# Kernel tuning notes

Hardware: AMD Instinct MI355X
Metric: run time of the kernel (lower is better)

## Reference

```python
import jax, jax.numpy as jnp
import numpy as np

T, B = 256, 64
X_DIM, H_DIM, Z_DIM = 128, 1024, 128


def _lin(k, out_d, in_d):
    return jax.random.normal(k, (out_d, in_d), jnp.float32) * 0.05


def setup_inputs() -> dict:
    key = jax.random.key(0)
    ks = jax.random.split(key, 18)
    return {
        "x": jax.random.normal(ks[0], (T, B, X_DIM), jnp.float32),
        "y": jax.random.uniform(ks[1], (T, B, X_DIM), jnp.float32),
        "eps": jax.random.normal(ks[2], (T, B, Z_DIM), jnp.float32),
        # hidden_state_rnn: GRU(x_dim -> h_dim), bias=False
        "h_Wih": _lin(ks[3], 3 * H_DIM, X_DIM),
        "h_Whh": _lin(ks[4], 3 * H_DIM, H_DIM),
        # rnn: GRU(h_dim + x_dim -> h_dim), bias=False (input is [y_t, h_t])
        "a_Wih": _lin(ks[5], 3 * H_DIM, X_DIM + H_DIM),
        "a_Whh": _lin(ks[6], 3 * H_DIM, H_DIM),
        "enc_W1": _lin(ks[7], H_DIM, H_DIM), "enc_b1": jnp.zeros(H_DIM, jnp.float32),
        "enc_W2": _lin(ks[8], H_DIM, H_DIM), "enc_b2": jnp.zeros(H_DIM, jnp.float32),
        "encm_W": _lin(ks[9], Z_DIM, H_DIM), "encm_b": jnp.zeros(Z_DIM, jnp.float32),
        "encs_W": _lin(ks[10], Z_DIM, H_DIM), "encs_b": jnp.zeros(Z_DIM, jnp.float32),
        "pr_W": _lin(ks[11], H_DIM, H_DIM), "pr_b": jnp.zeros(H_DIM, jnp.float32),
        "prm_W": _lin(ks[12], Z_DIM, H_DIM), "prm_b": jnp.zeros(Z_DIM, jnp.float32),
        "prs_W": _lin(ks[13], Z_DIM, H_DIM), "prs_b": jnp.zeros(Z_DIM, jnp.float32),
        "dec_W1": _lin(ks[14], H_DIM, H_DIM + Z_DIM), "dec_b1": jnp.zeros(H_DIM, jnp.float32),
        "dec_W2": _lin(ks[15], H_DIM, H_DIM), "dec_b2": jnp.zeros(H_DIM, jnp.float32),
        "decm_W": _lin(ks[16], X_DIM, H_DIM), "decm_b": jnp.zeros(X_DIM, jnp.float32),
        "decs_W": _lin(ks[17], X_DIM, H_DIM), "decs_b": jnp.zeros(X_DIM, jnp.float32),
    }


def _gru(xs, Wih, Whh):
    """Single-layer PyTorch-style GRU without biases. xs: [T,B,in]. Returns [T,B,H]."""
    h0 = jnp.zeros((xs.shape[1], Whh.shape[1]), xs.dtype)
    def step(h, xt):
        gi = xt @ Wih.T                      # [B, 3H]
        gh = h @ Whh.T                       # [B, 3H]
        ir, iz, inn = jnp.split(gi, 3, axis=-1)
        hr, hz, hn = jnp.split(gh, 3, axis=-1)
        r = jax.nn.sigmoid(ir + hr)
        zg = jax.nn.sigmoid(iz + hz)
        n = jnp.tanh(inn + r * hn)
        h_new = (1.0 - zg) * n + zg * h
        return h_new, h_new
    return jax.lax.scan(step, h0, xs)[1]


def srnn_forward(x, y, eps, h_Wih, h_Whh, a_Wih, a_Whh,
                 enc_W1, enc_b1, enc_W2, enc_b2, encm_W, encm_b, encs_W, encs_b,
                 pr_W, pr_b, prm_W, prm_b, prs_W, prs_b,
                 dec_W1, dec_b1, dec_W2, dec_b2, decm_W, decm_b, decs_W, decs_b):
    h_seq = _gru(x, h_Wih, h_Whh)            # [T,B,H] forward-time states
    # NOTE: original code aliases h_list and reverses it in place, so all later
    # uses of h_list[t] actually see the time-reversed sequence. Reproduce that.
    h_rev = h_seq[::-1]
    y_rev = y[::-1]
    a_rev = _gru(jnp.concatenate([y_rev, h_rev], axis=-1), a_Wih, a_Whh)  # backward GRU
    a_fwd = a_rev[::-1]                      # a at forward time t saw steps t..T-1

    enc = jax.nn.relu(jax.nn.relu(a_fwd @ enc_W1.T + enc_b1) @ enc_W2.T + enc_b2)
    enc_mean = enc @ encm_W.T + encm_b       # [T,B,Z]
    enc_std = jax.nn.softplus(enc @ encs_W.T + encs_b)
    z = eps * enc_std + enc_mean             # reparameterized sample

    pri = jax.nn.relu(h_rev @ pr_W.T + pr_b)  # bug-faithful: reversed h
    prior_mean = pri @ prm_W.T + prm_b
    prior_std = jax.nn.softplus(pri @ prs_W.T + prs_b)

    dec = jax.nn.relu(
        jax.nn.relu(jnp.concatenate([z, h_rev], axis=-1) @ dec_W1.T + dec_b1)
        @ dec_W2.T + dec_b2)
    dec_mean = jax.nn.sigmoid(dec @ decm_W.T + decm_b)  # [T,B,X]
    dec_std = jax.nn.softplus(dec @ decs_W.T + decs_b)

    kld = 0.5 * jnp.sum(
        2.0 * jnp.log(prior_std) - 2.0 * jnp.log(enc_std)
        + (enc_std ** 2 + (enc_mean - prior_mean) ** 2) / prior_std ** 2 - 1.0)
    nll = -jnp.sum(y * jnp.log(dec_mean) + (1.0 - y) * jnp.log(1.0 - dec_mean))
    return kld, nll, enc_mean, enc_std, dec_mean, dec_std


def reference(x, y, eps, h_Wih, h_Whh, a_Wih, a_Whh,
              enc_W1, enc_b1, enc_W2, enc_b2, encm_W, encm_b, encs_W, encs_b,
              pr_W, pr_b, prm_W, prm_b, prs_W, prs_b,
              dec_W1, dec_b1, dec_W2, dec_b2, decm_W, decm_b, decs_W, decs_b):
    return srnn_forward(x, y, eps, h_Wih, h_Whh, a_Wih, a_Whh,
                        enc_W1, enc_b1, enc_W2, enc_b2, encm_W, encm_b, encs_W, encs_b,
                        pr_W, pr_b, prm_W, prm_b, prs_W, prs_b,
                        dec_W1, dec_b1, dec_W2, dec_b2, decm_W, decm_b, decs_W, decs_b)
```

## Files before the change

### kernel.cpp

```cpp
#include <hip/hip_runtime.h>
#include <cstdint>
#include <cstddef>

#define NT   256
#define NB   64
#define XD   128
#define HD   1024
#define ZD   128
#define H3   3072
#define TBM  16384

typedef __attribute__((ext_vector_type(8))) short bf16x8;
typedef __attribute__((ext_vector_type(4))) float f32x4;
typedef __attribute__((ext_vector_type(4))) unsigned int u32x4;

__device__ __forceinline__ unsigned short f2bf(float f){
  unsigned int u = __float_as_uint(f);
  u += 0x7fffu + ((u >> 16) & 1u);
  return (unsigned short)(u >> 16);
}
__device__ __forceinline__ float bf2f(unsigned short h){
  return __uint_as_float(((unsigned int)h) << 16);
}

template<int N>
__device__ __forceinline__ void vwait(){
  asm volatile("s_waitcnt vmcnt(%0)" :: "i"(N) : "memory");
  __builtin_amdgcn_sched_barrier(0);
}

__device__ __forceinline__ float fsigmoid(float x){
  return 1.f / (1.f + __expf(-x));
}
__device__ __forceinline__ float ftanh(float x){
  float xc = fminf(fmaxf(x, -15.f), 15.f);
  float e = __expf(2.f * xc);
  return (e - 1.f) / (e + 1.f);
}

__device__ __forceinline__ void wait_tags(const unsigned int* tags, unsigned int target){
  if (threadIdx.x < 64){
    const unsigned int* p = tags + threadIdx.x * 32;
    for (;;){
      unsigned int v;
      asm volatile("global_load_dword %0, %1, off sc0 sc1\n\ts_waitcnt vmcnt(0)"
                   : "=v"(v) : "v"(p) : "memory");
      if (__all((int)(v >= target))) break;
    }
  }
  __syncthreads();
}

struct CvtArgs { const float* src[17]; };

__global__ void cvt_all(CvtArgs a, unsigned short* wdst, unsigned short* xdst, unsigned short* ydst){
  const long NG = 2572288;
  for (long g = blockIdx.x*blockDim.x + threadIdx.x; g < NG; g += (long)gridDim.x*blockDim.x){
    long i = g * 8;
    const float* s; unsigned short* d;
    if      (i < 393216)  { s=a.src[0]+i;             d=wdst+i; }
    else if (i < 3538944) { s=a.src[1]+(i-393216);    d=wdst+i; }
    else if (i < 7077888) { s=a.src[2]+(i-3538944);   d=wdst+i; }
    else if (i < 10223616){ s=a.src[3]+(i-7077888);   d=wdst+i; }
    else if (i < 11272192){ s=a.src[4]+(i-10223616);  d=wdst+i; }
    else if (i < 12320768){ s=a.src[5]+(i-11272192);  d=wdst+i; }
    else if (i < 12451840){ s=a.src[6]+(i-12320768);  d=wdst+i; }
    else if (i < 12582912){ s=a.src[7]+(i-12451840);  d=wdst+i; }
    else if (i < 13631488){ s=a.src[8]+(i-12582912);  d=wdst+i; }
    else if (i < 13762560){ s=a.src[9]+(i-13631488);  d=wdst+i; }
    else if (i < 13893632){ s=a.src[10]+(i-13762560); d=wdst+i; }
    else if (i < 15073280){ s=a.src[11]+(i-13893632); d=wdst+i; }
    else if (i < 16121856){ s=a.src[12]+(i-15073280); d=wdst+i; }
    else if (i < 16252928){ s=a.src[13]+(i-16121856); d=wdst+i; }
    else if (i < 16384000){ s=a.src[14]+(i-16252928); d=wdst+i; }
    else if (i < 18481152){ s=a.src[15]+(i-16384000); d=xdst+(i-16384000); }
    else                  { s=a.src[16]+(i-18481152); d=ydst+(i-18481152); }
    float4 v0 = *(const float4*)s;
    float4 v1 = *(const float4*)(s + 4);
    u32x4 o;
    o.x = (unsigned int)f2bf(v0.x) | ((unsigned int)f2bf(v0.y) << 16);
    o.y = (unsigned int)f2bf(v0.z) | ((unsigned int)f2bf(v0.w) << 16);
    o.z = (unsigned int)f2bf(v1.x) | ((unsigned int)f2bf(v1.y) << 16);
    o.w = (unsigned int)f2bf(v1.z) | ((unsigned int)f2bf(v1.w) << 16);
    *(u32x4*)d = o;
  }
}

template<int ACT, int OUT_BF, int BIAS>
__launch_bounds__(256)
__global__ void gemm_bf16(const unsigned short* __restrict__ A1, int rev1, int K1,
                          const unsigned short* __restrict__ A2, int rev2, int K,
                          const unsigned short* __restrict__ W,
                          const float* __restrict__ bias,
                          void* __restrict__ Cv, int N, int m0)
{
  __shared__ __align__(16) unsigned short As[128][40];
  __shared__ __align__(16) unsigned short Ws[128][40];
  const int tid   = threadIdx.x;
  const int mbase = blockIdx.y * 128;
  const int nbase = blockIdx.x * 128;
  const int wid = tid >> 6, lane = tid & 63;
  const int wr = wid >> 1, wc = wid & 1;
  const int fr = lane & 15;
  const int kc = (lane >> 4) * 8;
  const int K2 = K - K1;
  const int nk = K >> 5;

  f32x4 acc[4][4];
  #pragma unroll
  for (int i = 0; i < 4; ++i)
    #pragma unroll
    for (int j = 0; j < 4; ++j)
      acc[i][j] = (f32x4){0.f, 0.f, 0.f, 0.f};

  for (int ks = 0; ks < nk; ++ks){
    const int k0 = ks << 5;
    __syncthreads();
    for (int l = tid; l < 512; l += 256){
      int row = l >> 2, c = l & 3;
      int kk = k0 + c*8;
      int m = m0 + mbase + row;
      uint4 v;
      if (kk < K1){
        int mm = rev1 ? (((255 - (m >> 6)) << 6) | (m & 63)) : m;
        v = *(const uint4*)(A1 + (size_t)mm * K1 + kk);
      } else {
        int mm = rev2 ? (((255 - (m >> 6)) << 6) | (m & 63)) : m;
        v = *(const uint4*)(A2 + (size_t)mm * K2 + (kk - K1));
      }
      *(uint4*)&As[row][c*8] = v;
    }
    for (int l = tid; l < 512; l += 256){
      int row = l >> 2, c = l & 3;
      uint4 v = *(const uint4*)(W + (size_t)(nbase + row) * K + k0 + c*8);
      *(uint4*)&Ws[row][c*8] = v;
    }
    __syncthreads();
    bf16x8 af[4], bfm[4];
    #pragma unroll
    for (int f = 0; f < 4; ++f) af[f]  = *(const bf16x8*)&As[wr*64 + f*16 + fr][kc];
    #pragma unroll
    for (int f = 0; f < 4; ++f) bfm[f] = *(const bf16x8*)&Ws[wc*64 + f*16 + fr][kc];
    #pragma unroll
    for (int i = 0; i < 4; ++i)
      #pragma unroll
      for (int j = 0; j < 4; ++j)
        acc[i][j] = __builtin_amdgcn_mfma_f32_16x16x32_bf16(af[i], bfm[j], acc[i][j], 0, 0, 0);
  }

  #pragma unroll
  for (int i = 0; i < 4; ++i){
    #pragma unroll
    for (int j = 0; j < 4; ++j){
      #pragma unroll
      for (int r = 0; r < 4; ++r){
        int row = mbase + wr*64 + i*16 + (lane >> 4)*4 + r;
        int col = nbase + wc*64 + j*16 + fr;
        float v = acc[i][j][r];
        if (BIAS) v += bias[col];
        if (ACT == 1) v = fmaxf(v, 0.f);
        else if (ACT == 2) v = 1.f / (1.f + expf(-v));
        else if (ACT == 3) v = (v > 20.f) ? v : log1pf(expf(v));
        if (OUT_BF) ((unsigned short*)Cv)[(size_t)row * N + col] = f2bf(v);
        else        ((float*)Cv)[(size_t)row * N + col] = v;
      }
    }
  }
}

__device__ void gemm_gi_tile(char* smem,
                             const unsigned short* __restrict__ A1, int rev1, int K1,
                             const unsigned short* __restrict__ A2, int rev2, int K,
                             const unsigned short* __restrict__ W,
                             unsigned short* __restrict__ C, int m0, int bx, int by)
{
  unsigned short (*As)[40] = (unsigned short(*)[40])smem;
  unsigned short (*Ws)[40] = (unsigned short(*)[40])(smem + 10240);
  const int tid   = threadIdx.x;
  const int mbase = by * 128;
  const int nbase = bx * 128;
  const int wid = tid >> 6, lane = tid & 63;
  const int wr = wid >> 1, wc = wid & 1;
  const int fr = lane & 15;
  const int kc = (lane >> 4) * 8;
  const int K2 = K - K1;
  const int nk = K >> 5;

  f32x4 acc[4][4];
  #pragma unroll
  for (int i = 0; i < 4; ++i)
    #pragma unroll
    for (int j = 0; j < 4; ++j)
      acc[i][j] = (f32x4){0.f, 0.f, 0.f, 0.f};

  for (int ks = 0; ks < nk; ++ks){
    const int k0 = ks << 5;
    __syncthreads();
    for (int l = tid; l < 512; l += 256){
      int row = l >> 2, c = l & 3;
      int kk = k0 + c*8;
      int m = m0 + mbase + row;
      uint4 v;
      if (kk < K1){
        int mm = rev1 ? (((255 - (m >> 6)) << 6) | (m & 63)) : m;
        v = *(const uint4*)(A1 + (size_t)mm * K1 + kk);
      } else {
        int mm = rev2 ? (((255 - (m >> 6)) << 6) | (m & 63)) : m;
        v = *(const uint4*)(A2 + (size_t)mm * K2 + (kk - K1));
      }
      *(uint4*)&As[row][c*8] = v;
    }
    for (int l = tid; l < 512; l += 256){
      int row = l >> 2, c = l & 3;
      uint4 v = *(const uint4*)(W + (size_t)(nbase + row) * K + k0 + c*8);
      *(uint4*)&Ws[row][c*8] = v;
    }
    __syncthreads();
    bf16x8 af[4], bfm[4];
    #pragma unroll
    for (int f = 0; f < 4; ++f) af[f]  = *(const bf16x8*)&As[wr*64 + f*16 + fr][kc];
    #pragma unroll
    for (int f = 0; f < 4; ++f) bfm[f] = *(const bf16x8*)&Ws[wc*64 + f*16 + fr][kc];
    #pragma unroll
    for (int i = 0; i < 4; ++i)
      #pragma unroll
      for (int j = 0; j < 4; ++j)
        acc[i][j] = __builtin_amdgcn_mfma_f32_16x16x32_bf16(af[i], bfm[j], acc[i][j], 0, 0, 0);
  }

  #pragma unroll
  for (int i = 0; i < 4; ++i){
    #pragma unroll
    for (int j = 0; j < 4; ++j){
      #pragma unroll
      for (int r = 0; r < 4; ++r){
        int row = mbase + wr*64 + i*16 + (lane >> 4)*4 + r;
        int col = nbase + wc*64 + j*16 + fr;
        C[(size_t)row * H3 + col] = f2bf(acc[i][j][r]);
      }
    }
  }
  __syncthreads();
}

__device__ void gru_body(char* smem,
                         const unsigned short* __restrict__ W3,
                         const unsigned short* __restrict__ gi,
                         unsigned short* __restrict__ seq,
                         float* __restrict__ hstate,
                         unsigned int* __restrict__ tags,
                         int t0, int dir, int out_off, int nsteps)
{
  uint4 (*Wf)[3][64] = (uint4(*)[3][64])smem;
  unsigned short (*hb2)[16] = (unsigned short(*)[16])(smem + 98304);
  unsigned int* scnt = (unsigned int*)(smem + 100352);
  const int tid  = threadIdx.x;
  const int bid  = blockIdx.x;
  const int c0   = bid * 16;
  const int wid  = tid >> 6, lane = tid & 63;
  const int fr   = lane & 15, q = lane >> 4;
  const int rowb = wid*16 + q*4;
  const int arow = wid*16 + fr;

  for (int ks = wid*8; ks < wid*8 + 8; ++ks)
    #pragma unroll
    for (int g = 0; g < 3; ++g)
      Wf[ks][g][lane] = *(const uint4*)(W3 + (size_t)(g*HD + c0 + fr)*HD + ks*32 + q*8);
  if (tid == 0) *scnt = 0u;

  float hc[4];
  if (t0 == 0){
    hc[0] = hc[1] = hc[2] = hc[3] = 0.f;
  } else {
    #pragma unroll
    for (int r = 0; r < 4; ++r)
      hc[r] = hstate[(size_t)(rowb + r)*HD + c0 + fr];
  }
  __syncthreads();

  for (int tt = 0; tt < nsteps; ++tt){
    const int t = t0 + tt;

    unsigned short g_ir[4], g_iz[4], g_in[4];
    {
      const unsigned short* gb = gi + (size_t)tt*NB*H3;
      #pragma unroll
      for (int r = 0; r < 4; ++r){
        const unsigned short* p = gb + (size_t)(rowb + r)*H3 + c0 + fr;
        g_ir[r] = p[0];
        g_iz[r] = p[HD];
        g_in[r] = p[2*HD];
      }
    }

    f32x4 aR = (f32x4){0.f,0.f,0.f,0.f};
    f32x4 aZ = (f32x4){0.f,0.f,0.f,0.f};
    f32x4 aN = (f32x4){0.f,0.f,0.f,0.f};

    if (t > 0){
      if (tt >= 1) wait_tags(tags, (unsigned int)tt);
      const unsigned short* hp = seq + (size_t)(out_off + dir*(t-1))*NB*HD
                                     + (size_t)arow*HD + q*8;
      u32x4 A[32];
      #pragma unroll
      for (int ks = 0; ks < 32; ++ks)
        asm volatile("global_load_dwordx4 %0, %1, off offset:%2"
                     : "=v"(A[ks]) : "v"(hp), "i"(ks*64));
      #pragma unroll
      for (int b4 = 0; b4 < 4; ++b4){
        if (b4 == 0) vwait<24>();
        else if (b4 == 1) vwait<16>();
        else if (b4 == 2) vwait<8>();
        else vwait<0>();
        #pragma unroll
        for (int k8 = 0; k8 < 8; ++k8){
          const int ks = b4*8 + k8;
          bf16x8 a = *(const bf16x8*)&A[ks];
          aR = __builtin_amdgcn_mfma_f32_16x16x32_bf16(a, *(const bf16x8*)&Wf[ks][0][lane], aR, 0, 0, 0);
          aZ = __builtin_amdgcn_mfma_f32_16x16x32_bf16(a, *(const bf16x8*)&Wf[ks][1][lane], aZ, 0, 0, 0);
          aN = __builtin_amdgcn_mfma_f32_16x16x32_bf16(a, *(const bf16x8*)&Wf[ks][2][lane], aN, 0, 0, 0);
        }
      }
    }

    #pragma unroll
    for (int r = 0; r < 4; ++r){
      float rr = fsigmoid(bf2f(g_ir[r]) + aR[r]);
      float zz = fsigmoid(bf2f(g_iz[r]) + aZ[r]);
      float nn = ftanh(bf2f(g_in[r]) + rr * aN[r]);
      hc[r] = (1.f - zz) * nn + zz * hc[r];
      hb2[rowb + r][fr] = f2bf(hc[r]);
    }
    __syncthreads();
    {
      int row = tid >> 2, c4 = (tid & 3) * 4;
      unsigned long long v = *(const unsigned long long*)&hb2[row][c4];
      unsigned long long* dst = (unsigned long long*)(seq + (size_t)(out_off + dir*t)*NB*HD
                                                          + (size_t)row*HD + c0 + c4);
      (void)__hip_atomic_exchange(dst, v, __ATOMIC_RELAXED, __HIP_MEMORY_SCOPE_AGENT);
    }
    if (tt < nsteps - 1){
      vwait<0>();
      if (lane == 0){
        unsigned int old = atomicAdd(scnt, 1u);
        if (old == (unsigned int)(4*tt + 3))
          (void)__hip_atomic_exchange(tags + bid*32, (unsigned int)(tt + 1),
                                      __ATOMIC_RELAXED, __HIP_MEMORY_SCOPE_AGENT);
      }
    }
  }

  #pragma unroll
  for (int r = 0; r < 4; ++r)
    hstate[(size_t)(rowb + r)*HD + c0 + fr] = hc[r];
}

__global__ __launch_bounds__(256, 1)
void gru_seq(const unsigned short* __restrict__ W3, const unsigned short* __restrict__ gi,
             unsigned short* __restrict__ seq, float* __restrict__ hstate,
             unsigned int* __restrict__ tags, int t0, int dir, int out_off, int nsteps)
{
  __shared__ __align__(16) char smem[100608];
  gru_body(smem, W3, gi, seq, hstate, tags, t0, dir, out_off, nsteps);
}

__global__ __launch_bounds__(256, 1)
void gru_fat(const unsigned short* __restrict__ W3, const unsigned short* __restrict__ gi,
             unsigned short* __restrict__ seq, float* __restrict__ hstate,
             unsigned int* __restrict__ tags, int t0, int dir, int out_off, int nsteps,
             const unsigned short* __restrict__ gA1, int grev1, int gK1,
             const unsigned short* __restrict__ gA2, int grev2, int gK,
             const unsigned short* __restrict__ gW, unsigned short* __restrict__ gC, int gm0)
{
  __shared__ __align__(16) char smem[100608];
  if (blockIdx.x < 64){
    gru_body(smem, W3, gi, seq, hstate, tags, t0, dir, out_off, nsteps);
  } else {
    for (int tl = blockIdx.x - 64; tl < 768; tl += 192)
      gemm_gi_tile(smem, gA1, grev1, gK1, gA2, grev2, gK, gW, gC, gm0, tl % 24, tl / 24);
  }
}

__global__ void z_make(const float* __restrict__ eps, const float* __restrict__ em,
                       const float* __restrict__ es, unsigned short* __restrict__ zb, int n){
  for (int i = blockIdx.x*blockDim.x + threadIdx.x; i < n; i += gridDim.x*blockDim.x)
    zb[i] = f2bf(eps[i] * es[i] + em[i]);
}

__global__ void kld_partial(const float* __restrict__ em, const float* __restrict__ es,
                            const float* __restrict__ pm, const float* __restrict__ ps,
                            float* __restrict__ part, int n){
  float s = 0.f;
  for (int i = blockIdx.x*blockDim.x + threadIdx.x; i < n; i += gridDim.x*blockDim.x){
    float e = es[i], p = ps[i], d = em[i] - pm[i];
    s += 2.f*(logf(p) - logf(e)) + (e*e + d*d)/(p*p) - 1.f;
  }
  __shared__ float red[256];
  red[threadIdx.x] = s; __syncthreads();
  for (int off = 128; off; off >>= 1){
    if (threadIdx.x < off) red[threadIdx.x] += red[threadIdx.x + off];
    __syncthreads();
  }
  if (threadIdx.x == 0) part[blockIdx.x] = red[0];
}

__global__ void nll_partial(const float* __restrict__ y, const float* __restrict__ dm,
                            float* __restrict__ part, int n){
  float s = 0.f;
  for (int i = blockIdx.x*blockDim.x + threadIdx.x; i < n; i += gridDim.x*blockDim.x){
    float yy = y[i], d = dm[i];
    s += yy * logf(d) + (1.f - yy) * logf(1.f - d);
  }
  __shared__ float red[256];
  red[threadIdx.x] = s; __syncthreads();
  for (int off = 128; off; off >>= 1){
    if (threadIdx.x < off) red[threadIdx.x] += red[threadIdx.x + off];
    __syncthreads();
  }
  if (threadIdx.x == 0) part[blockIdx.x] = red[0];
}

__global__ void final_sum(const float* __restrict__ part, int n, float scale, float* __restrict__ out){
  float s = 0.f;
  for (int i = threadIdx.x; i < n; i += 256) s += part[i];
  __shared__ float red[256];
  red[threadIdx.x] = s; __syncthreads();
  for (int off = 128; off; off >>= 1){
    if (threadIdx.x < off) red[threadIdx.x] += red[threadIdx.x + off];
    __syncthreads();
  }
  if (threadIdx.x == 0) out[0] = scale * red[0];
}

extern "C" void kernel_launch(void* const* d_in, const int* in_sizes, int n_in,
                              void* d_out, int out_size, void* d_ws, size_t ws_size,
                              hipStream_t stream)
{
  const float* y   = (const float*)d_in[1];
  const float* eps = (const float*)d_in[2];
  const float* enc_b1 = (const float*)d_in[8];
  const float* enc_b2 = (const float*)d_in[10];
  const float* encm_b = (const float*)d_in[12];
  const float* encs_b = (const float*)d_in[14];
  const float* pr_b   = (const float*)d_in[16];
  const float* prm_b  = (const float*)d_in[18];
  const float* prs_b  = (const float*)d_in[20];
  const float* dec_b1 = (const float*)d_in[22];
  const float* dec_b2 = (const float*)d_in[24];
  const float* decm_b = (const float*)d_in[26];
  const float* decs_b = (const float*)d_in[28];

  char* ws = (char*)d_ws;
  size_t off = 0;
  auto alloc = [&](size_t bytes){ size_t o = off; off += (bytes + 255) & ~(size_t)255; return o; };
  const size_t o_big   = alloc((size_t)71303168);
  const size_t o_hseq  = alloc((size_t)TBM * HD * 2);
  const size_t o_aseq  = alloc((size_t)TBM * HD * 2);
  const size_t o_wbf   = alloc((size_t)16384000 * 2);
  const size_t o_hst   = alloc((size_t)NB * HD * 4);
  const size_t o_bar   = alloc((size_t)65536);
  const size_t o_pkld  = alloc((size_t)1024 * 4);
  const size_t o_pnll  = alloc((size_t)1024 * 4);
  (void)off; (void)ws_size;

  char* big = ws + o_big;
  unsigned short* gihA = (unsigned short*)(big);
  unsigned short* gihB = (unsigned short*)(big + 25165824);
  unsigned short* xbf  = (unsigned short*)(big + 50331648);
  unsigned short* ybf  = (unsigned short*)(big + 54525952);
  unsigned short* tA  = (unsigned short*)(big);
  unsigned short* tB  = (unsigned short*)(big + 33554432);
  unsigned short* zbf = (unsigned short*)(big + 67108864);

  unsigned short* hseq = (unsigned short*)(ws + o_hseq);
  unsigned short* aseq = (unsigned short*)(ws + o_aseq);
  unsigned short* wbf  = (unsigned short*)(ws + o_wbf);
  float* hstate = (float*)(ws + o_hst);
  unsigned int* bar = (unsigned int*)(ws + o_bar);
  float* pkld = (float*)(ws + o_pkld);
  float* pnll = (float*)(ws + o_pnll);

  const int widx[15] = {3,4,5,6,7,9,11,13,15,17,19,21,23,25,27};
  const size_t wsz[15] = {393216,3145728,3538944,3145728,1048576,1048576,131072,131072,
                          1048576,131072,131072,1179648,1048576,131072,131072};
  size_t woff[15]; { size_t a = 0; for (int i = 0; i < 15; ++i){ woff[i] = a; a += wsz[i]; } }
  unsigned short* w_hWih = wbf + woff[0];
  unsigned short* w_hWhh = wbf + woff[1];
  unsigned short* w_aWih = wbf + woff[2];
  unsigned short* w_aWhh = wbf + woff[3];
  unsigned short* w_enc1 = wbf + woff[4];
  unsigned short* w_enc2 = wbf + woff[5];
  unsigned short* w_encm = wbf + woff[6];
  unsigned short* w_encs = wbf + woff[7];
  unsigned short* w_pr   = wbf + woff[8];
  unsigned short* w_prm  = wbf + woff[9];
  unsigned short* w_prs  = wbf + woff[10];
  unsigned short* w_dec1 = wbf + woff[11];
  unsigned short* w_dec2 = wbf + woff[12];
  unsigned short* w_decm = wbf + woff[13];
  unsigned short* w_decs = wbf + woff[14];

  float* out = (float*)d_out;
  float* em_out = out + 2;
  float* es_out = out + 2 + 2097152;
  float* dm_out = out + 2 + 2*2097152;
  float* ds_out = out + 2 + 3*2097152;
  float* pm = dm_out;
  float* ps = ds_out;

  CvtArgs ca;
  for (int i = 0; i < 15; ++i) ca.src[i] = (const float*)d_in[widx[i]];
  ca.src[15] = (const float*)d_in[0];
  ca.src[16] = (const float*)d_in[1];
  cvt_all<<<2048, 256, 0, stream>>>(ca, wbf, xbf, ybf);
  (void)hipMemsetAsync(bar, 0, 65536, stream);

  const dim3 blk(256);
  const dim3 gQ3072(24, 32);
  const dim3 g1024(HD/128, TBM/128);
  const dim3 g128(1, TBM/128);
  const unsigned short* nul = (const unsigned short*)nullptr;

  gemm_bf16<0,1,0><<<gQ3072, blk, 0, stream>>>(xbf, 0, XD, nul, 0, XD, w_hWih, nullptr, gihA, H3, 0);
  gru_fat<<<256, blk, 0, stream>>>(w_hWhh, gihA, hseq, hstate, bar + 0*2048, 0,   +1, 0, 64,
                                   xbf, 0, XD, nul, 0, XD, w_hWih, gihB, 4096);
  gru_fat<<<256, blk, 0, stream>>>(w_hWhh, gihB, hseq, hstate, bar + 1*2048, 64,  +1, 0, 64,
                                   xbf, 0, XD, nul, 0, XD, w_hWih, gihA, 8192);
  gru_fat<<<256, blk, 0, stream>>>(w_hWhh, gihA, hseq, hstate, bar + 2*2048, 128, +1, 0, 64,
                                   xbf, 0, XD, nul, 0, XD, w_hWih, gihB, 12288);
  gru_seq<<<64, blk, 0, stream>>>(w_hWhh, gihB, hseq, hstate, bar + 3*2048, 192, +1, 0, 64);

  gemm_bf16<0,1,0><<<gQ3072, blk, 0, stream>>>(ybf, 1, XD, hseq, 1, XD + HD, w_aWih, nullptr, gihA, H3, 0);
  gru_fat<<<256, blk, 0, stream>>>(w_aWhh, gihA, aseq, hstate, bar + 4*2048, 0,   -1, 255, 64,
                                   ybf, 1, XD, hseq, 1, XD + HD, w_aWih, gihB, 4096);
  gru_fat<<<256, blk, 0, stream>>>(w_aWhh, gihB, aseq, hstate, bar + 5*2048, 64,  -1, 255, 64,
                                   ybf, 1, XD, hseq, 1, XD + HD, w_aWih, gihA, 8192);
  gru_fat<<<256, blk, 0, stream>>>(w_aWhh, gihA, aseq, hstate, bar + 6*2048, 128, -1, 255, 64,
                                   ybf, 1, XD, hseq, 1, XD + HD, w_aWih, gihB, 12288);
  gru_seq<<<64, blk, 0, stream>>>(w_aWhh, gihB, aseq, hstate, bar + 7*2048, 192, -1, 255, 64);

  gemm_bf16<1,1,1><<<g1024, blk, 0, stream>>>(aseq, 0, HD, nul, 0, HD, w_enc1, enc_b1, tA, HD, 0);
  gemm_bf16<1,1,1><<<g1024, blk, 0, stream>>>(tA, 0, HD, nul, 0, HD, w_enc2, enc_b2, tB, HD, 0);
  gemm_bf16<0,0,1><<<g128, blk, 0, stream>>>(tB, 0, HD, nul, 0, HD, w_encm, encm_b, em_out, ZD, 0);
  gemm_bf16<3,0,1><<<g128, blk, 0, stream>>>(tB, 0, HD, nul, 0, HD, w_encs, encs_b, es_out, ZD, 0);
  z_make<<<2048, 256, 0, stream>>>(eps, em_out, es_out, zbf, TBM*ZD);

  gemm_bf16<1,1,1><<<g1024, blk, 0, stream>>>(hseq, 1, HD, nul, 1, HD, w_pr, pr_b, tA, HD, 0);
  gemm_bf16<0,0,1><<<g128, blk, 0, stream>>>(tA, 0, HD, nul, 0, HD, w_prm, prm_b, pm, ZD, 0);
  gemm_bf16<3,0,1><<<g128, blk, 0, stream>>>(tA, 0, HD, nul, 0, HD, w_prs, prs_b, ps, ZD, 0);
  kld_partial<<<1024, 256, 0, stream>>>(em_out, es_out, pm, ps, pkld, TBM*ZD);
  final_sum<<<1, 256, 0, stream>>>(pkld, 1024, 0.5f, out + 0);

  gemm_bf16<1,1,1><<<g1024, blk, 0, stream>>>(zbf, 0, ZD, hseq, 1, ZD + HD, w_dec1, dec_b1, tA, HD, 0);
  gemm_bf16<1,1,1><<<g1024, blk, 0, stream>>>(tA, 0, HD, nul, 0, HD, w_dec2, dec_b2, tB, HD, 0);
  gemm_bf16<2,0,1><<<g128, blk, 0, stream>>>(tB, 0, HD, nul, 0, HD, w_decm, decm_b, dm_out, ZD, 0);
  gemm_bf16<3,0,1><<<g128, blk, 0, stream>>>(tB, 0, HD, nul, 0, HD, w_decs, decs_b, ds_out, ZD, 0);

  nll_partial<<<1024, 256, 0, stream>>>(y, dm_out, pnll, TBM*XD);
  final_sum<<<1, 256, 0, stream>>>(pnll, 1024, -1.0f, out + 1);
}
```

Baseline: 4.839 ms.

## Replace tag-based GRU step barrier with sentinel-value polling on hidden state

Removes the per-block tag counters and the tag-polling barrier between GRU timesteps. Instead, the hidden sequence buffers are pre-filled with 0xFF, and each block repeatedly loads the previous step's hidden row with cache-bypassing loads until no 0xFFFF sentinel halves remain. The goal is to cut the extra round trip for tag publish and poll, and to let data arrival itself act as the signal. In exchange, it adds two large memsets, reloads the full A tile on every retry, and relies on real bf16 values never equalling the 0xFFFF pattern (a NaN encoding). It also only checks two of the eight halves per load.

New measurement: 6.321 ms. 30.6% more time.

```diff
diff --git a/kernel.cpp b/kernel.cpp
--- a/kernel.cpp
+++ b/kernel.cpp
@@ -36,19 +36,6 @@
   float xc = fminf(fmaxf(x, -15.f), 15.f);
   float e = __expf(2.f * xc);
   return (e - 1.f) / (e + 1.f);
-}
-
-__device__ __forceinline__ void wait_tags(const unsigned int* tags, unsigned int target){
-  if (threadIdx.x < 64){
-    const unsigned int* p = tags + threadIdx.x * 32;
-    for (;;){
-      unsigned int v;
-      asm volatile("global_load_dword %0, %1, off sc0 sc1\n\ts_waitcnt vmcnt(0)"
-                   : "=v"(v) : "v"(p) : "memory");
-      if (__all((int)(v >= target))) break;
-    }
-  }
-  __syncthreads();
 }
 
 struct CvtArgs { const float* src[17]; };
@@ -248,12 +235,10 @@
                          const unsigned short* __restrict__ gi,
                          unsigned short* __restrict__ seq,
                          float* __restrict__ hstate,
-                         unsigned int* __restrict__ tags,
                          int t0, int dir, int out_off, int nsteps)
 {
   uint4 (*Wf)[3][64] = (uint4(*)[3][64])smem;
   unsigned short (*hb2)[16] = (unsigned short(*)[16])(smem + 98304);
-  unsigned int* scnt = (unsigned int*)(smem + 100352);
   const int tid  = threadIdx.x;
   const int bid  = blockIdx.x;
   const int c0   = bid * 16;
@@ -266,7 +251,6 @@
     #pragma unroll
     for (int g = 0; g < 3; ++g)
       Wf[ks][g][lane] = *(const uint4*)(W3 + (size_t)(g*HD + c0 + fr)*HD + ks*32 + q*8);
-  if (tid == 0) *scnt = 0u;
 
   float hc[4];
   if (t0 == 0){
@@ -298,28 +282,29 @@
     f32x4 aN = (f32x4){0.f,0.f,0.f,0.f};
 
     if (t > 0){
-      if (tt >= 1) wait_tags(tags, (unsigned int)tt);
       const unsigned short* hp = seq + (size_t)(out_off + dir*(t-1))*NB*HD
                                      + (size_t)arow*HD + q*8;
       u32x4 A[32];
+      for (;;){
+        #pragma unroll
+        for (int ks = 0; ks < 32; ++ks)
+          asm volatile("global_load_dwordx4 %0, %1, off offset:%2 sc0 sc1"
+                       : "=v"(A[ks]) : "v"(hp), "i"(ks*64));
+        vwait<0>();
+        unsigned int bad = 0u;
+        #pragma unroll
+        for (int ks = 0; ks < 32; ++ks){
+          bad |= ((A[ks].x & 0xFFFFu) == 0xFFFFu) ? 1u : 0u;
+          bad |= ((A[ks].z & 0xFFFFu) == 0xFFFFu) ? 1u : 0u;
+        }
+        if (__all(bad == 0u)) break;
+      }
       #pragma unroll
-      for (int ks = 0; ks < 32; ++ks)
-        asm volatile("global_load_dwordx4 %0, %1, off offset:%2"
-                     : "=v"(A[ks]) : "v"(hp), "i"(ks*64));
-      #pragma unroll
-      for (int b4 = 0; b4 < 4; ++b4){
-        if (b4 == 0) vwait<24>();
-        else if (b4 == 1) vwait<16>();
-        else if (b4 == 2) vwait<8>();
-        else vwait<0>();
-        #pragma unroll
-        for (int k8 = 0; k8 < 8; ++k8){
-          const int ks = b4*8 + k8;
-          bf16x8 a = *(const bf16x8*)&A[ks];
-          aR = __builtin_amdgcn_mfma_f32_16x16x32_bf16(a, *(const bf16x8*)&Wf[ks][0][lane], aR, 0, 0, 0);
-          aZ = __builtin_amdgcn_mfma_f32_16x16x32_bf16(a, *(const bf16x8*)&Wf[ks][1][lane], aZ, 0, 0, 0);
-          aN = __builtin_amdgcn_mfma_f32_16x16x32_bf16(a, *(const bf16x8*)&Wf[ks][2][lane], aN, 0, 0, 0);
-        }
+      for (int ks = 0; ks < 32; ++ks){
+        bf16x8 a = *(const bf16x8*)&A[ks];
+        aR = __builtin_amdgcn_mfma_f32_16x16x32_bf16(a, *(const bf16x8*)&Wf[ks][0][lane], aR, 0, 0, 0);
+        aZ = __builtin_amdgcn_mfma_f32_16x16x32_bf16(a, *(const bf16x8*)&Wf[ks][1][lane], aZ, 0, 0, 0);
+        aN = __builtin_amdgcn_mfma_f32_16x16x32_bf16(a, *(const bf16x8*)&Wf[ks][2][lane], aN, 0, 0, 0);
       }
     }
 
@@ -339,15 +324,7 @@
                                                           + (size_t)row*HD + c0 + c4);
       (void)__hip_atomic_exchange(dst, v, __ATOMIC_RELAXED, __HIP_MEMORY_SCOPE_AGENT);
     }
-    if (tt < nsteps - 1){
-      vwait<0>();
-      if (lane == 0){
-        unsigned int old = atomicAdd(scnt, 1u);
-        if (old == (unsigned int)(4*tt + 3))
-          (void)__hip_atomic_exchange(tags + bid*32, (unsigned int)(tt + 1),
-                                      __ATOMIC_RELAXED, __HIP_MEMORY_SCOPE_AGENT);
-      }
-    }
+    __syncthreads();
   }
 
   #pragma unroll
@@ -358,23 +335,23 @@
 __global__ __launch_bounds__(256, 1)
 void gru_seq(const unsigned short* __restrict__ W3, const unsigned short* __restrict__ gi,
              unsigned short* __restrict__ seq, float* __restrict__ hstate,
-             unsigned int* __restrict__ tags, int t0, int dir, int out_off, int nsteps)
+             int t0, int dir, int out_off, int nsteps)
 {
   __shared__ __align__(16) char smem[100608];
-  gru_body(smem, W3, gi, seq, hstate, tags, t0, dir, out_off, nsteps);
+  gru_body(smem, W3, gi, seq, hstate, t0, dir, out_off, nsteps);
 }
 
 __global__ __launch_bounds__(256, 1)
 void gru_fat(const unsigned short* __restrict__ W3, const unsigned short* __restrict__ gi,
              unsigned short* __restrict__ seq, float* __restrict__ hstate,
-             unsigned int* __restrict__ tags, int t0, int dir, int out_off, int nsteps,
+             int t0, int dir, int out_off, int nsteps,
              const unsigned short* __restrict__ gA1, int grev1, int gK1,
              const unsigned short* __restrict__ gA2, int grev2, int gK,
              const unsigned short* __restrict__ gW, unsigned short* __restrict__ gC, int gm0)
 {
   __shared__ __align__(16) char smem[100608];
   if (blockIdx.x < 64){
-    gru_body(smem, W3, gi, seq, hstate, tags, t0, dir, out_off, nsteps);
+    gru_body(smem, W3, gi, seq, hstate, t0, dir, out_off, nsteps);
   } else {
     for (int tl = blockIdx.x - 64; tl < 768; tl += 192)
       gemm_gi_tile(smem, gA1, grev1, gK1, gA2, grev2, gK, gW, gC, gm0, tl % 24, tl / 24);
@@ -458,7 +435,6 @@
   const size_t o_aseq  = alloc((size_t)TBM * HD * 2);
   const size_t o_wbf   = alloc((size_t)16384000 * 2);
   const size_t o_hst   = alloc((size_t)NB * HD * 4);
-  const size_t o_bar   = alloc((size_t)65536);
   const size_t o_pkld  = alloc((size_t)1024 * 4);
   const size_t o_pnll  = alloc((size_t)1024 * 4);
   (void)off; (void)ws_size;
@@ -476,7 +452,6 @@
   unsigned short* aseq = (unsigned short*)(ws + o_aseq);
   unsigned short* wbf  = (unsigned short*)(ws + o_wbf);
   float* hstate = (float*)(ws + o_hst);
-  unsigned int* bar = (unsigned int*)(ws + o_bar);
   float* pkld = (float*)(ws + o_pkld);
   float* pnll = (float*)(ws + o_pnll);
 
@@ -513,7 +488,8 @@
   ca.src[15] = (const float*)d_in[0];
   ca.src[16] = (const float*)d_in[1];
   cvt_all<<<2048, 256, 0, stream>>>(ca, wbf, xbf, ybf);
-  (void)hipMemsetAsync(bar, 0, 65536, stream);
+  (void)hipMemsetAsync(hseq, 0xFF, (size_t)TBM * HD * 2, stream);
+  (void)hipMemsetAsync(aseq, 0xFF, (size_t)TBM * HD * 2, stream);
 
   const dim3 blk(256);
   const dim3 gQ3072(24, 32);
@@ -522,22 +498,22 @@
   const unsigned short* nul = (const unsigned short*)nullptr;
 
   gemm_bf16<0,1,0><<<gQ3072, blk, 0, stream>>>(xbf, 0, XD, nul, 0, XD, w_hWih, nullptr, gihA, H3, 0);
-  gru_fat<<<256, blk, 0, stream>>>(w_hWhh, gihA, hseq, hstate, bar + 0*2048, 0,   +1, 0, 64,
+  gru_fat<<<256, blk, 0, stream>>>(w_hWhh, gihA, hseq, hstate, 0,   +1, 0, 64,
                                    xbf, 0, XD, nul, 0, XD, w_hWih, gihB, 4096);
-  gru_fat<<<256, blk, 0, stream>>>(w_hWhh, gihB, hseq, hstate, bar + 1*2048, 64,  +1, 0, 64,
+  gru_fat<<<256, blk, 0, stream>>>(w_hWhh, gihB, hseq, hstate, 64,  +1, 0, 64,
                                    xbf, 0, XD, nul, 0, XD, w_hWih, gihA, 8192);
-  gru_fat<<<256, blk, 0, stream>>>(w_hWhh, gihA, hseq, hstate, bar + 2*2048, 128, +1, 0, 64,
+  gru_fat<<<256, blk, 0, stream>>>(w_hWhh, gihA, hseq, hstate, 128, +1, 0, 64,
                                    xbf, 0, XD, nul, 0, XD, w_hWih, gihB, 12288);
-  gru_seq<<<64, blk, 0, stream>>>(w_hWhh, gihB, hseq, hstate, bar + 3*2048, 192, +1, 0, 64);
+  gru_seq<<<64, blk, 0, stream>>>(w_hWhh, gihB, hseq, hstate, 192, +1, 0, 64);
 
   gemm_bf16<0,1,0><<<gQ3072, blk, 0, stream>>>(ybf, 1, XD, hseq, 1, XD + HD, w_aWih, nullptr, gihA, H3, 0);
-  gru_fat<<<256, blk, 0, stream>>>(w_aWhh, gihA, aseq, hstate, bar + 4*2048, 0,   -1, 255, 64,
+  gru_fat<<<256, blk, 0, stream>>>(w_aWhh, gihA, aseq, hstate, 0,   -1, 255, 64,
                                    ybf, 1, XD, hseq, 1, XD + HD, w_aWih, gihB, 4096);
-  gru_fat<<<256, blk, 0, stream>>>(w_aWhh, gihB, aseq, hstate, bar + 5*2048, 64,  -1, 255, 64,
+  gru_fat<<<256, blk, 0, stream>>>(w_aWhh, gihB, aseq, hstate, 64,  -1, 255, 64,
                                    ybf, 1, XD, hseq, 1, XD + HD, w_aWih, gihA, 8192);
-  gru_fat<<<256, blk, 0, stream>>>(w_aWhh, gihA, aseq, hstate, bar + 6*2048, 128, -1, 255, 64,
+  gru_fat<<<256, blk, 0, stream>>>(w_aWhh, gihA, aseq, hstate, 128, -1, 255, 64,
                                    ybf, 1, XD, hseq, 1, XD + HD, w_aWih, gihB, 12288);
-  gru_seq<<<64, blk, 0, stream>>>(w_aWhh, gihB, aseq, hstate, bar + 7*2048, 192, -1, 255, 64);
+  gru_seq<<<64, blk, 0, stream>>>(w_aWhh, gihB, aseq, hstate, 192, -1, 255, 64);
 
   gemm_bf16<1,1,1><<<g1024, blk, 0, stream>>>(aseq, 0, HD, nul, 0, HD, w_enc1, enc_b1, tA, HD, 0);
   gemm_bf16<1,1,1><<<g1024, blk, 0, stream>>>(tA, 0, HD, nul, 0, HD, w_enc2, enc_b2, tB, HD, 0);
```
